# Kernel optimization log

Hardware: AMD Instinct MI355X
Metric: run time of the kernel (lower is better)

Reference implementation:

```python
import jax, jax.numpy as jnp
import numpy as np

N_NODES = 8192
N_EDGES = 65536
NB = 10            # number_of_basis
MID = 32           # middle_layer_size
MAX_R = 10.0       # max_radius
NZ, NM = 48, 16    # z / mol embedding sizes -> 64x0e node input
IN_S = NZ + NM     # 64 scalars
H_S, H_V = 32, 8   # hidden irreps 32x0e + 8x1o (dim 56)
O_S = 16           # output irreps 16x0e
W0N = IN_S * H_S + IN_S * H_V                                  # 2560
W1N = H_S*H_S + H_V*H_S + H_S*H_V + H_V*H_V + H_V*H_V          # 1664
W2N = H_S*O_S + H_V*O_S                                        # 640
H_DIM = H_S + 3 * H_V                                          # 56


def _fcnet(e, W1, W2):
    # e3nn FullyConnectedNet([NB, MID, numel], silu): fan-in normalized linears
    h = jax.nn.silu(e @ W1 / np.sqrt(W1.shape[0]))
    return h @ W2 / np.sqrt(W2.shape[0])


def _ln(x, g, b):
    m = jnp.mean(x, -1, keepdims=True)
    v = jnp.var(x, -1, keepdims=True)
    return (x - m) * jax.lax.rsqrt(v + 1e-5) * g + b


def _sus(t):
    # smooth compact-support bump helper: exp(-1/t) for t>0 else 0
    return jnp.where(t > 0, jnp.exp(-1.0 / jnp.where(t > 0, t, 1.0)), 0.0)


def _forward(pos, Ez, Em,
             b0_W1, b0_W2, b0_g, b0_b,
             b1_W1, b1_W2, b1_g, b1_b,
             b2_W1, b2_W2, b2_g, b2_b,
             z, mol_id, edge_src, edge_dst):
    N = pos.shape[0]
    E = edge_src.shape[0]
    avg = E / N  # avg_num_neighbors (static)

    # node embedding: 64x0e
    x = jnp.concatenate([Ez[z], Em[mol_id]], axis=-1)          # [N, 64]

    vec = pos[edge_dst] - pos[edge_src]                        # [E, 3]
    length = jnp.linalg.norm(vec, axis=1)                      # [E]

    # soft_one_hot_linspace(basis='smooth_finite', cutoff=True) * sqrt(NB)
    vals = jnp.linspace(0.0, MAX_R, NB + 2)[1:-1]
    step = MAX_R / (NB + 1)
    u = (length[:, None] - vals) / step
    emb = (1.14136 * np.exp(2.0)) * _sus(u + 1.0) * _sus(1.0 - u)
    emb = emb * np.sqrt(NB)                                    # [E, NB]

    # spherical harmonics lmax=1, normalize=True, 'component' norm
    nrm = vec / jnp.maximum(length, 1e-9)[:, None]
    sh_v = np.sqrt(3.0) * nrm                                  # [E, 3]  (l=1; l=0 comp == 1)

    # ---- interaction block 0: 64x0e -> 32x0e + 8x1o ----
    w = _fcnet(emb, b0_W1, b0_W2)                              # [E, 2560]
    w00 = w[:, :IN_S * H_S].reshape(E, IN_S, H_S)
    w01 = w[:, IN_S * H_S:].reshape(E, IN_S, H_V)
    xe = x[edge_src]                                           # [E, 64]
    es = jnp.einsum('eu,euw->ew', xe, w00) / np.sqrt(IN_S)
    ev = jnp.einsum('eu,euw,ei->ewi', xe, w01, sh_v) / np.sqrt(IN_S)
    msg = jnp.concatenate([es, ev.reshape(E, 3 * H_V)], -1)    # [E, 56]
    x = _ln(jax.ops.segment_sum(msg, edge_dst, num_segments=N) / np.sqrt(avg), b0_g, b0_b)

    # ---- interaction block 1: 32x0e+8x1o -> 32x0e+8x1o ----
    w = _fcnet(emb, b1_W1, b1_W2)                              # [E, 1664]
    o = 0
    w_ss  = w[:, o:o + H_S*H_S].reshape(E, H_S, H_S); o += H_S*H_S
    w_vvs = w[:, o:o + H_V*H_S].reshape(E, H_V, H_S); o += H_V*H_S
    w_sv  = w[:, o:o + H_S*H_V].reshape(E, H_S, H_V); o += H_S*H_V
    w_vs  = w[:, o:o + H_V*H_V].reshape(E, H_V, H_V); o += H_V*H_V
    w_vvv = w[:, o:o + H_V*H_V].reshape(E, H_V, H_V)
    xs = x[:, :H_S][edge_src]                                  # [E, 32]
    xv = x[:, H_S:].reshape(N, H_V, 3)[edge_src]               # [E, 8, 3]
    dot = jnp.einsum('eui,ei->eu', xv, sh_v) / np.sqrt(3.0)    # 1o x 1o -> 0e CG
    crs = jnp.cross(xv, sh_v[:, None, :]) / np.sqrt(2.0)       # 1o x 1o -> 1o CG
    es = (jnp.einsum('eu,euw->ew', xs, w_ss) / np.sqrt(H_S)
          + jnp.einsum('eu,euw->ew', dot, w_vvs) / np.sqrt(H_V)) / np.sqrt(2.0)
    ev = (jnp.einsum('eu,euw,ei->ewi', xs, w_sv, sh_v) / np.sqrt(H_S)
          + jnp.einsum('eui,euw->ewi', xv, w_vs) / np.sqrt(H_V)
          + jnp.einsum('eui,euw->ewi', crs, w_vvv) / np.sqrt(H_V)) / np.sqrt(3.0)
    msg = jnp.concatenate([es, ev.reshape(E, 3 * H_V)], -1)
    x = _ln(jax.ops.segment_sum(msg, edge_dst, num_segments=N) / np.sqrt(avg), b1_g, b1_b)

    # ---- interaction block 2: 32x0e+8x1o -> 16x0e ----
    w = _fcnet(emb, b2_W1, b2_W2)                              # [E, 640]
    w_ss  = w[:, :H_S * O_S].reshape(E, H_S, O_S)
    w_vvs = w[:, H_S * O_S:].reshape(E, H_V, O_S)
    xs = x[:, :H_S][edge_src]
    xv = x[:, H_S:].reshape(N, H_V, 3)[edge_src]
    dot = jnp.einsum('eui,ei->eu', xv, sh_v) / np.sqrt(3.0)
    es = (jnp.einsum('eu,euw->ew', xs, w_ss) / np.sqrt(H_S)
          + jnp.einsum('eu,euw->ew', dot, w_vvs) / np.sqrt(H_V)) / np.sqrt(2.0)
    x = _ln(jax.ops.segment_sum(es, edge_dst, num_segments=N) / np.sqrt(avg), b2_g, b2_b)
    return x                                                   # [N, 16]


def setup_inputs():
    key = jax.random.key(0)
    ks = jax.random.split(key, 16)
    edge_src = jax.random.randint(ks[3], (N_EDGES,), 0, N_NODES)
    # exclude self-loops (radius_graph never returns them)
    edge_dst = (edge_src + 1 + jax.random.randint(ks[4], (N_EDGES,), 0, N_NODES - 1)) % N_NODES
    return {
        'pos': jax.random.uniform(ks[0], (N_NODES, 3), jnp.float32) * 8.0,
        'z': jax.random.randint(ks[1], (N_NODES,), 0, 100),
        'mol_id': jax.random.randint(ks[2], (N_NODES,), 0, 2),
        'edge_src': edge_src,
        'edge_dst': edge_dst,
        'Ez': jax.random.normal(ks[5], (100, NZ), jnp.float32),
        'Em': jax.random.normal(ks[6], (2, NM), jnp.float32),
        'b0_W1': jax.random.normal(ks[7], (NB, MID), jnp.float32),
        'b0_W2': jax.random.normal(ks[8], (MID, W0N), jnp.float32),
        'b0_g': jnp.ones((H_DIM,), jnp.float32),
        'b0_b': jnp.zeros((H_DIM,), jnp.float32),
        'b1_W1': jax.random.normal(ks[9], (NB, MID), jnp.float32),
        'b1_W2': jax.random.normal(ks[10], (MID, W1N), jnp.float32),
        'b1_g': jnp.ones((H_DIM,), jnp.float32),
        'b1_b': jnp.zeros((H_DIM,), jnp.float32),
        'b2_W1': jax.random.normal(ks[11], (NB, MID), jnp.float32),
        'b2_W2': jax.random.normal(ks[12], (MID, W2N), jnp.float32),
        'b2_g': jnp.ones((O_S,), jnp.float32),
        'b2_b': jnp.zeros((O_S,), jnp.float32),
    }


def reference(pos, z, mol_id, edge_src, edge_dst, Ez, Em,
              b0_W1, b0_W2, b0_g, b0_b,
              b1_W1, b1_W2, b1_g, b1_b,
              b2_W1, b2_W2, b2_g, b2_b):
    return _forward(pos, Ez, Em,
                    b0_W1, b0_W2, b0_g, b0_b,
                    b1_W1, b1_W2, b1_g, b1_b,
                    b2_W1, b2_W2, b2_g, b2_b,
                    z, mol_id, edge_src, edge_dst)
```

## Files before the change

### kernel.cpp

```cpp
#include <hip/hip_runtime.h>

#define NNODES 8192
#define NEDGES 65536

#define K_PACK   0.02209708691f
#define K_P1SV   0.01804219593f
#define K_VVS    0.04419417382f
#define K_VS     0.03608439182f
#define K_VVV    0.02551551815f
#define K_DOT    0.57735026919f
#define K_PRELN  0.35355339059f
#define C_EMB    8.4335730689f

typedef unsigned int uint32;
typedef unsigned short ushort16;
typedef __attribute__((ext_vector_type(8))) short short8;
typedef __attribute__((ext_vector_type(4))) float floatx4;

__device__ __forceinline__ float siluf(float x) { return x / (1.0f + __expf(-x)); }
__device__ __forceinline__ float susf(float t) { return t > 0.0f ? __expf(-1.0f / t) : 0.0f; }
__device__ __forceinline__ ushort16 f2bf(float f) {
  uint32 u = __float_as_uint(f);
  return (ushort16)((u + 0x7fffu + ((u >> 16) & 1u)) >> 16);
}
__device__ __forceinline__ float bflo(uint32 v) { return __uint_as_float(v << 16); }
__device__ __forceinline__ float bfhi(uint32 v) { return __uint_as_float(v & 0xffff0000u); }
__device__ __forceinline__ float bfs(ushort16 v) { return __uint_as_float((uint32)v << 16); }

__global__ __launch_bounds__(256) void k_prep(
    const float* __restrict__ pos, const int* __restrict__ z, const int* __restrict__ mol,
    const int* __restrict__ esrc, const int* __restrict__ edst,
    const float* __restrict__ Ez, const float* __restrict__ Em,
    const float* __restrict__ W10, const float* __restrict__ W11, const float* __restrict__ W12,
    const float* __restrict__ W20, const float* __restrict__ W21, const float* __restrict__ W22,
    int* __restrict__ combo, ushort16* __restrict__ X0cb, float* __restrict__ sh,
    ushort16* __restrict__ h0b, ushort16* __restrict__ h1b, ushort16* __restrict__ h2b,
    ushort16* __restrict__ Bp0, ushort16* __restrict__ Bp1, ushort16* __restrict__ Bp2,
    ushort16* __restrict__ Bpw1, ushort16* __restrict__ Bpw2,
    int* __restrict__ deg, int* __restrict__ eidx) {
  __shared__ float Wl[320];
  int b = blockIdx.x;
  if (b < 768) {
    int which = b >> 8;
    int e = ((b & 255) << 8) + threadIdx.x;
    const float* W = (which == 0) ? W10 : (which == 1) ? W11 : W12;
    for (int i = threadIdx.x; i < 320; i += 256) Wl[i] = W[i];
    __syncthreads();
    int s = esrc[e], d = edst[e];
    float vx = pos[d * 3 + 0] - pos[s * 3 + 0];
    float vy = pos[d * 3 + 1] - pos[s * 3 + 1];
    float vz = pos[d * 3 + 2] - pos[s * 3 + 2];
    float len = sqrtf(vx * vx + vy * vy + vz * vz);
    if (which == 0) {
      int p = atomicAdd(&deg[d], 1);
      if (p < 64) eidx[(size_t)d * 64 + p] = e;
      float inv = 1.7320508076f / fmaxf(len, 1e-9f);
      sh[e * 3 + 0] = vx * inv; sh[e * 3 + 1] = vy * inv; sh[e * 3 + 2] = vz * inv;
    }
    float emb[10];
#pragma unroll
    for (int k = 0; k < 10; ++k) {
      float u = len * 1.1f - (float)(k + 1);
      emb[k] = C_EMB * susf(u + 1.0f) * susf(1.0f - u);
    }
    float H[32];
#pragma unroll
    for (int m = 0; m < 32; ++m) {
      float t = 0.f;
#pragma unroll
      for (int k = 0; k < 10; ++k) t += emb[k] * Wl[k * 32 + m];
      H[m] = siluf(t);
    }
    ushort16* hb = (which == 0) ? h0b : (which == 1) ? h1b : h2b;
    uint32* hp = (uint32*)(hb + (size_t)e * 32);
#pragma unroll
    for (int m = 0; m < 16; ++m)
      hp[m] = (uint32)f2bf(H[2 * m]) | ((uint32)f2bf(H[2 * m + 1]) << 16);
    return;
  }
  int idx = (b - 768) * 256 + threadIdx.x;
  if (idx < NNODES) { combo[idx] = z[idx] * 2 + mol[idx]; return; }
  idx -= NNODES;
  if (idx < 16384) {
    int c = idx >> 6, j = idx & 63;
    float v = 0.f;
    if (c < 200) {
      int zz = c >> 1, mm = c & 1;
      v = (j < 48) ? Ez[zz * 48 + j] : Em[mm * 16 + (j - 48)];
    }
    X0cb[idx] = f2bf(v);
    return;
  }
  idx -= 16384;
  if (idx < 81920) {
    int tile = idx >> 10; int r = idx & 1023;
    int kh = r >> 9; int rr = r & 511;
    int lane = rr >> 3, j = rr & 7;
    int k = kh * 32 + (lane >> 4) * 8 + j;
    int n = tile * 16 + (lane & 15);
    int c = n >> 5, m = n & 31;
    int col = (c < 32) ? (k * 32 + c) : (2048 + k * 8 + (c - 32));
    Bp0[idx] = f2bf(W20[m * 2560 + col] * K_PACK);
    return;
  }
  idx -= 81920;
  if (idx < 40960) {
    int tile = idx >> 9; int rr = idx & 511;
    int lane = rr >> 3, j = rr & 7;
    int k = (lane >> 4) * 8 + j;
    int n = tile * 16 + (lane & 15);
    int c = n >> 5, m = n & 31;
    float v = (c < 32) ? W21[m * 1664 + k * 32 + c] * K_PACK
                       : W21[m * 1664 + 1280 + k * 8 + (c - 32)] * K_P1SV;
    Bp1[idx] = f2bf(v);
    return;
  }
  idx -= 40960;
  if (idx < 16384) {
    int tile = idx >> 9; int rr = idx & 511;
    int lane = rr >> 3, j = rr & 7;
    int k = (lane >> 4) * 8 + j;
    int n = tile * 16 + (lane & 15);
    int c = n >> 5, m = n & 31;
    Bp2[idx] = f2bf(W22[m * 640 + k * 16 + c] * K_PACK);
    return;
  }
  idx -= 16384;
  if (idx < 12288) {
    int tile = idx >> 9; int rr = idx & 511;
    int lane = rr >> 3, j = rr & 7;
    int m = (lane >> 4) * 8 + j;
    int n = tile * 16 + (lane & 15);
    float v;
    if (n < 256) {
      int c = n >> 3, u = n & 7;
      v = W21[m * 1664 + 1024 + u * 32 + c] * K_VVS;
    } else if (n < 320) {
      int vo = (n - 256) >> 3, u = n & 7;
      v = W21[m * 1664 + 1536 + u * 8 + vo] * K_VS;
    } else {
      int vo = (n - 320) >> 3, u = n & 7;
      v = W21[m * 1664 + 1600 + u * 8 + vo] * K_VVV;
    }
    Bpw1[idx] = f2bf(v);
    return;
  }
  idx -= 12288;
  {
    int tile = idx >> 9; int rr = idx & 511;
    int lane = rr >> 3, j = rr & 7;
    int m = (lane >> 4) * 8 + j;
    int n = tile * 16 + (lane & 15);
    int c = n >> 3, u = n & 7;
    Bpw2[idx] = f2bf(W22[m * 640 + 512 + u * 16 + c] * K_VVS);
  }
}

__device__ __forceinline__ void gemm_tile(
    const ushort16* __restrict__ A, const ushort16* __restrict__ Bp, ushort16* __restrict__ C,
    int N, int K, int bx, int by, int wave, int lane) {
  int m0 = bx * 64 + wave * 16;
  int n0 = by * 64;
  int row = lane & 15, q = lane >> 4;
  int nkh = K >> 5;
  floatx4 acc[4];
  floatx4 zero = {0.f, 0.f, 0.f, 0.f};
#pragma unroll
  for (int t = 0; t < 4; ++t) acc[t] = zero;
  for (int kh = 0; kh < nkh; ++kh) {
    short8 a = *reinterpret_cast<const short8*>(A + (size_t)(m0 + row) * K + kh * 32 + q * 8);
#pragma unroll
    for (int t = 0; t < 4; ++t) {
      int T = (n0 >> 4) + t;
      short8 b = *reinterpret_cast<const short8*>(Bp + ((size_t)T * nkh + kh) * 512 + lane * 8);
      acc[t] = __builtin_amdgcn_mfma_f32_16x16x32_bf16(a, b, acc[t], 0, 0, 0);
    }
  }
  int colb = n0 + row;
#pragma unroll
  for (int t = 0; t < 4; ++t)
#pragma unroll
    for (int r = 0; r < 4; ++r)
      C[(size_t)(m0 + q * 4 + r) * N + colb + t * 16] = f2bf(acc[t][r]);
}

__global__ __launch_bounds__(256) void k_gemm_mfma(
    const ushort16* __restrict__ A, const ushort16* __restrict__ Bp, ushort16* __restrict__ C,
    int N, int K) {
  gemm_tile(A, Bp, C, N, K, blockIdx.x, blockIdx.y, threadIdx.x >> 6, threadIdx.x & 63);
}

__global__ __launch_bounds__(256) void k_gather0(
    const int* __restrict__ deg, const int* __restrict__ eidx,
    const int* __restrict__ combo, const int* __restrict__ esrc,
    const float* __restrict__ sh, const ushort16* __restrict__ hb,
    const ushort16* __restrict__ Pb,
    const float* __restrict__ g, const float* __restrict__ b,
    ushort16* __restrict__ xsb, float* __restrict__ xvf) {
  int n = __builtin_amdgcn_readfirstlane(blockIdx.x * 4 + (threadIdx.x >> 6));
  int lane = threadIdx.x & 63;
  int row = lane & 15, q = lane >> 4;
  int cnt = deg[n]; if (cnt > 64) cnt = 64;
  const int* ep = eidx + (size_t)n * 64;
  int lv = lane - 32;
  int vq = (lv >= 0) ? ((lv / 3 > 7) ? 7 : lv / 3) : 0;
  int vi = (lv >= 0) ? (lv - (lv / 3) * 3) : 0;
  int c2 = 32 + row; if (c2 > 39) c2 = 39;
  floatx4 zero = {0.f, 0.f, 0.f, 0.f};
  float v = 0.f;
  for (int j = 0; j < cnt; ++j) {
    int e = __builtin_amdgcn_readfirstlane(ep[j]);
    int s = __builtin_amdgcn_readfirstlane(esrc[e]);
    int rp = __builtin_amdgcn_readfirstlane(combo[s]);
    float sh0 = sh[e * 3 + 0], sh1 = sh[e * 3 + 1], sh2 = sh[e * 3 + 2];
    short8 af = *reinterpret_cast<const short8*>(hb + (size_t)e * 32 + q * 8);
    const ushort16* Pr = Pb + (size_t)rp * 1280;
    short8 bf0 = *reinterpret_cast<const short8*>(Pr + row * 32 + q * 8);
    short8 bf1 = *reinterpret_cast<const short8*>(Pr + (16 + row) * 32 + q * 8);
    short8 bf2 = *reinterpret_cast<const short8*>(Pr + c2 * 32 + q * 8);
    floatx4 p0 = __builtin_amdgcn_mfma_f32_16x16x32_bf16(af, bf0, zero, 0, 0, 0);
    floatx4 p1 = __builtin_amdgcn_mfma_f32_16x16x32_bf16(af, bf1, zero, 0, 0, 0);
    floatx4 p2 = __builtin_amdgcn_mfma_f32_16x16x32_bf16(af, bf2, zero, 0, 0, 0);
    float pv2 = __shfl(p2[0], vq, 64);
    float pdot = (lane < 16) ? p0[0] : (lane < 32) ? p1[0] : pv2;
    float mult = (lane < 32) ? 1.0f : ((vi == 0) ? sh0 : (vi == 1) ? sh1 : sh2);
    v += pdot * mult;
  }
  v *= K_PRELN;
  if (lane >= 56) v = 0.f;
  float sm = v, sq = v * v;
#pragma unroll
  for (int off = 32; off > 0; off >>= 1) {
    sm += __shfl_xor(sm, off, 64);
    sq += __shfl_xor(sq, off, 64);
  }
  float invD = 1.0f / 56.0f;
  float mean = sm * invD;
  float var = sq * invD - mean * mean;
  float rs = rsqrtf(var + 1e-5f);
  float r = (v - mean) * rs * g[lane < 56 ? lane : 0] + b[lane < 56 ? lane : 0];
  if (lane < 32) xsb[(size_t)n * 32 + lane] = f2bf(r);
  else if (lane < 56) xvf[(size_t)n * 24 + lane - 32] = r;
}

__global__ __launch_bounds__(256) void k_msg1f(
    const int* __restrict__ esrc, const float* __restrict__ sh, const ushort16* __restrict__ hb,
    const ushort16* __restrict__ Pb, const float* __restrict__ xv,
    const ushort16* __restrict__ Bpw, ushort16* __restrict__ msg) {
  __shared__ ushort16 Wlds[16][392];
  int w = threadIdx.x >> 6, lane = threadIdx.x & 63;
  int e0 = __builtin_amdgcn_readfirstlane(blockIdx.x * 16);
  int row = lane & 15, q = lane >> 4;
  short8 a1 = *reinterpret_cast<const short8*>(hb + (size_t)(e0 + row) * 32 + q * 8);
  floatx4 zero = {0.f, 0.f, 0.f, 0.f};
#pragma unroll
  for (int t6 = 0; t6 < 6; ++t6) {
    int T = w * 6 + t6;
    short8 b1 = *reinterpret_cast<const short8*>(Bpw + (size_t)T * 512 + lane * 8);
    floatx4 acc = __builtin_amdgcn_mfma_f32_16x16x32_bf16(a1, b1, zero, 0, 0, 0);
#pragma unroll
    for (int r = 0; r < 4; ++r)
      Wlds[q * 4 + r][T * 16 + row] = f2bf(acc[r]);
  }
  __syncthreads();
  int lv = lane - 32;
  int vq = (lv >= 0) ? ((lv / 3 > 7) ? 7 : lv / 3) : 0;
  int vi = (lv >= 0) ? (lv - (lv / 3) * 3) : 0;
  int c2 = 32 + row; if (c2 > 39) c2 = 39;
#pragma unroll
  for (int k = 0; k < 4; ++k) {
    int e = e0 + w * 4 + k;
    int s = __builtin_amdgcn_readfirstlane(esrc[e]);
    float sh0 = sh[e * 3 + 0], sh1 = sh[e * 3 + 1], sh2 = sh[e * 3 + 2];
    const float* xr = xv + (size_t)s * 24;
    const ushort16* wp = &Wlds[w * 4 + k][0];
    float vterm, mult;
    if (lane < 32) {
      mult = 1.0f;
      uint4 wv = *reinterpret_cast<const uint4*>(wp + lane * 8);
      float ww[8] = {bflo(wv.x), bfhi(wv.x), bflo(wv.y), bfhi(wv.y),
                     bflo(wv.z), bfhi(wv.z), bflo(wv.w), bfhi(wv.w)};
      vterm = 0.f;
#pragma unroll
      for (int u = 0; u < 8; ++u) {
        float du = K_DOT * (xr[u * 3] * sh0 + xr[u * 3 + 1] * sh1 + xr[u * 3 + 2] * sh2);
        vterm += du * ww[u];
      }
    } else {
      float shi = (vi == 0) ? sh0 : (vi == 1) ? sh1 : sh2;
      float s1 = (vi == 0) ? sh1 : (vi == 1) ? sh2 : sh0;
      float s2 = (vi == 0) ? sh2 : (vi == 1) ? sh0 : sh1;
      mult = shi;
      uint4 wvs = *reinterpret_cast<const uint4*>(wp + 256 + vq * 8);
      uint4 wvv = *reinterpret_cast<const uint4*>(wp + 320 + vq * 8);
      float vsw[8] = {bflo(wvs.x), bfhi(wvs.x), bflo(wvs.y), bfhi(wvs.y),
                      bflo(wvs.z), bfhi(wvs.z), bflo(wvs.w), bfhi(wvs.w)};
      float vvw[8] = {bflo(wvv.x), bfhi(wvv.x), bflo(wvv.y), bfhi(wvv.y),
                      bflo(wvv.z), bfhi(wvv.z), bflo(wvv.w), bfhi(wvv.w)};
      vterm = 0.f;
#pragma unroll
      for (int u = 0; u < 8; ++u) {
        float xu0 = xr[u * 3], xu1 = xr[u * 3 + 1], xu2 = xr[u * 3 + 2];
        float xui = (vi == 0) ? xu0 : (vi == 1) ? xu1 : xu2;
        float xi1 = (vi == 0) ? xu1 : (vi == 1) ? xu2 : xu0;
        float xi2 = (vi == 0) ? xu2 : (vi == 1) ? xu0 : xu1;
        float crs = xi1 * s2 - xi2 * s1;
        vterm += xui * vsw[u] + crs * vvw[u];
      }
    }
    short8 af = *reinterpret_cast<const short8*>(hb + (size_t)e * 32 + q * 8);
    const ushort16* Pr = Pb + (size_t)s * 1280;
    short8 bf0 = *reinterpret_cast<const short8*>(Pr + row * 32 + q * 8);
    short8 bf1 = *reinterpret_cast<const short8*>(Pr + (16 + row) * 32 + q * 8);
    short8 bf2 = *reinterpret_cast<const short8*>(Pr + c2 * 32 + q * 8);
    floatx4 p0 = __builtin_amdgcn_mfma_f32_16x16x32_bf16(af, bf0, zero, 0, 0, 0);
    floatx4 p1 = __builtin_amdgcn_mfma_f32_16x16x32_bf16(af, bf1, zero, 0, 0, 0);
    floatx4 p2 = __builtin_amdgcn_mfma_f32_16x16x32_bf16(af, bf2, zero, 0, 0, 0);
    float pv2 = __shfl(p2[0], vq, 64);
    float pdot = (lane < 16) ? p0[0] : (lane < 32) ? p1[0] : pv2;
    if (lane < 56) msg[(size_t)e * 56 + lane] = f2bf(pdot * mult + vterm);
  }
}

__global__ __launch_bounds__(256) void k_msg2f(
    const int* __restrict__ esrc, const float* __restrict__ sh, const ushort16* __restrict__ hb,
    const ushort16* __restrict__ Pb, const float* __restrict__ xv,
    const ushort16* __restrict__ Bpw, ushort16* __restrict__ msg) {
  __shared__ ushort16 Wlds[16][136];
  int w = threadIdx.x >> 6, lane = threadIdx.x & 63;
  int e0 = __builtin_amdgcn_readfirstlane(blockIdx.x * 16);
  int row = lane & 15, q = lane >> 4;
  short8 a1 = *reinterpret_cast<const short8*>(hb + (size_t)(e0 + row) * 32 + q * 8);
  floatx4 zero = {0.f, 0.f, 0.f, 0.f};
#pragma unroll
  for (int t2 = 0; t2 < 2; ++t2) {
    int T = w * 2 + t2;
    short8 b1 = *reinterpret_cast<const short8*>(Bpw + (size_t)T * 512 + lane * 8);
    floatx4 acc = __builtin_amdgcn_mfma_f32_16x16x32_bf16(a1, b1, zero, 0, 0, 0);
#pragma unroll
    for (int r = 0; r < 4; ++r)
      Wlds[q * 4 + r][T * 16 + row] = f2bf(acc[r]);
  }
  __syncthreads();
  int cch = lane & 15;
#pragma unroll
  for (int k = 0; k < 4; ++k) {
    int e = e0 + w * 4 + k;
    int s = __builtin_amdgcn_readfirstlane(esrc[e]);
    float sh0 = sh[e * 3 + 0], sh1 = sh[e * 3 + 1], sh2 = sh[e * 3 + 2];
    const float* xr = xv + (size_t)s * 24;
    uint4 wv = *reinterpret_cast<const uint4*>(&Wlds[w * 4 + k][0] + cch * 8);
    float ww[8] = {bflo(wv.x), bfhi(wv.x), bflo(wv.y), bfhi(wv.y),
                   bflo(wv.z), bfhi(wv.z), bflo(wv.w), bfhi(wv.w)};
    float vterm = 0.f;
#pragma unroll
    for (int u = 0; u < 8; ++u) {
      float du = K_DOT * (xr[u * 3] * sh0 + xr[u * 3 + 1] * sh1 + xr[u * 3 + 2] * sh2);
      vterm += du * ww[u];
    }
    short8 af = *reinterpret_cast<const short8*>(hb + (size_t)e * 32 + q * 8);
    short8 bf = *reinterpret_cast<const short8*>(Pb + (size_t)s * 512 + row * 32 + q * 8);
    floatx4 p0 = __builtin_amdgcn_mfma_f32_16x16x32_bf16(af, bf, zero, 0, 0, 0);
    if (lane < 16) msg[(size_t)e * 16 + lane] = f2bf(p0[0] + vterm);
  }
}

__global__ __launch_bounds__(256) void k_gather_ln(
    const int* __restrict__ deg, const int* __restrict__ eidx,
    const ushort16* __restrict__ msg, int D,
    const float* __restrict__ g, const float* __restrict__ b,
    ushort16* __restrict__ xsb, float* __restrict__ xvf, float* __restrict__ outf) {
  int n = __builtin_amdgcn_readfirstlane(blockIdx.x * 4 + (threadIdx.x >> 6));
  int lane = threadIdx.x & 63;
  int cnt = deg[n]; if (cnt > 64) cnt = 64;
  const int* ep = eidx + (size_t)n * 64;
  float v = 0.f;
  for (int j = 0; j < cnt; ++j) {
    int e = ep[j];
    if (lane < D) v += bfs(msg[(size_t)e * D + lane]);
  }
  v *= K_PRELN;
  if (lane >= D) v = 0.f;
  float sm = v, sq = v * v;
#pragma unroll
  for (int off = 32; off > 0; off >>= 1) {
    sm += __shfl_xor(sm, off, 64);
    sq += __shfl_xor(sq, off, 64);
  }
  float invD = 1.0f / (float)D;
  float mean = sm * invD;
  float var = sq * invD - mean * mean;
  float rs = rsqrtf(var + 1e-5f);
  float r = (v - mean) * rs * g[lane < D ? lane : 0] + b[lane < D ? lane : 0];
  if (outf) {
    if (lane < D) outf[(size_t)n * D + lane] = r;
  } else {
    if (lane < 32) xsb[(size_t)n * 32 + lane] = f2bf(r);
    else if (lane < 56) xvf[(size_t)n * 24 + lane - 32] = r;
  }
}

extern "C" void kernel_launch(void* const* d_in, const int* in_sizes, int n_in,
                              void* d_out, int out_size, void* d_ws, size_t ws_size,
                              hipStream_t stream) {
  const float* pos = (const float*)d_in[0];
  const int* z = (const int*)d_in[1];
  const int* mol = (const int*)d_in[2];
  const int* esrc = (const int*)d_in[3];
  const int* edst = (const int*)d_in[4];
  const float* Ez = (const float*)d_in[5];
  const float* Em = (const float*)d_in[6];
  const float* b0W1 = (const float*)d_in[7];
  const float* b0W2 = (const float*)d_in[8];
  const float* b0g = (const float*)d_in[9];
  const float* b0b = (const float*)d_in[10];
  const float* b1W1 = (const float*)d_in[11];
  const float* b1W2 = (const float*)d_in[12];
  const float* b1g = (const float*)d_in[13];
  const float* b1b = (const float*)d_in[14];
  const float* b2W1 = (const float*)d_in[15];
  const float* b2W2 = (const float*)d_in[16];
  const float* b2g = (const float*)d_in[17];
  const float* b2b = (const float*)d_in[18];
  float* out = (float*)d_out;

  float* ws = (float*)d_ws;
  size_t o = 0;
  int* combo = (int*)(ws + o); o += NNODES;
  int* deg = (int*)(ws + o); o += NNODES;
  int* eidx = (int*)(ws + o); o += (size_t)NNODES * 64;
  ushort16* X0cb = (ushort16*)(ws + o); o += 8192;
  ushort16* xs1b = (ushort16*)(ws + o); o += 131072;
  float* xv1 = ws + o; o += (size_t)NNODES * 24;
  ushort16* h0b = (ushort16*)(ws + o); o += (size_t)NEDGES * 16;
  ushort16* h1b = (ushort16*)(ws + o); o += (size_t)NEDGES * 16;
  ushort16* h2b = (ushort16*)(ws + o); o += (size_t)NEDGES * 16;
  float* shb = ws + o; o += (size_t)NEDGES * 3;
  ushort16* Bp0 = (ushort16*)(ws + o); o += 40960;
  ushort16* Bp1 = (ushort16*)(ws + o); o += 20480;
  ushort16* Bp2 = (ushort16*)(ws + o); o += 8192;
  ushort16* Bpw1 = (ushort16*)(ws + o); o += 6144;
  ushort16* Bpw2 = (ushort16*)(ws + o); o += 2048;
  ushort16* P12 = (ushort16*)(ws + o); o += (size_t)NNODES * 640;
  ushort16* msgb = (ushort16*)(ws + o); o += (size_t)NEDGES * 28;

  ushort16* P0c = P12;
  ushort16* xs2b = xs1b;
  float* xv2 = xv1;
  ushort16* msg16 = msgb;

  hipMemsetAsync(deg, 0, NNODES * sizeof(int), stream);

  k_prep<<<1472, 256, 0, stream>>>(pos, z, mol, esrc, edst, Ez, Em,
                                   b0W1, b1W1, b2W1, b0W2, b1W2, b2W2,
                                   combo, X0cb, shb, h0b, h1b, h2b,
                                   Bp0, Bp1, Bp2, Bpw1, Bpw2, deg, eidx);

  k_gemm_mfma<<<dim3(4, 20), 256, 0, stream>>>(X0cb, Bp0, P0c, 1280, 64);
  k_gather0<<<2048, 256, 0, stream>>>(deg, eidx, combo, esrc, shb, h0b, P0c,
                                      b0g, b0b, xs1b, xv1);

  k_gemm_mfma<<<dim3(128, 20), 256, 0, stream>>>(xs1b, Bp1, P12, 1280, 32);
  k_msg1f<<<4096, 256, 0, stream>>>(esrc, shb, h1b, P12, xv1, Bpw1, msgb);
  k_gather_ln<<<2048, 256, 0, stream>>>(deg, eidx, msgb, 56, b1g, b1b, xs2b, xv2, nullptr);

  k_gemm_mfma<<<dim3(128, 8), 256, 0, stream>>>(xs2b, Bp2, P12, 512, 32);
  k_msg2f<<<4096, 256, 0, stream>>>(esrc, shb, h2b, P12, xv2, Bpw2, msg16);
  k_gather_ln<<<2048, 256, 0, stream>>>(deg, eidx, msg16, 16, b2g, b2b, nullptr, nullptr, out);
}
```

Measured before the change: 205.3 us.

## Fuse block-2 message computation into destination-node gather and layer norm

Replaces the per-edge k_msg2f kernel and the following k_gather_ln pass with one kernel, k_gather2. Each wave walks one destination node's incoming edges, computes each message in registers and accumulates it, then applies the final layer norm and writes the output. This removes the bf16 message buffer's write and re-read and one kernel launch. In exchange it adds eight small MFMAs per edge (the Bpw2 layout is repacked for this) and serialises per-node edge work inside a wave, where it was batched across edges before.

```diff
diff --git a/kernel.cpp b/kernel.cpp
--- a/kernel.cpp
+++ b/kernel.cpp
@@ -150,9 +150,8 @@
     int tile = idx >> 9; int rr = idx & 511;
     int lane = rr >> 3, j = rr & 7;
     int m = (lane >> 4) * 8 + j;
-    int n = tile * 16 + (lane & 15);
-    int c = n >> 3, u = n & 7;
-    Bpw2[idx] = f2bf(W22[m * 640 + 512 + u * 16 + c] * K_VVS);
+    int c = lane & 15;
+    Bpw2[idx] = f2bf(W22[m * 640 + 512 + tile * 16 + c] * K_VVS);
   }
 }
 
@@ -322,47 +321,57 @@
   }
 }
 
-__global__ __launch_bounds__(256) void k_msg2f(
-    const int* __restrict__ esrc, const float* __restrict__ sh, const ushort16* __restrict__ hb,
-    const ushort16* __restrict__ Pb, const float* __restrict__ xv,
-    const ushort16* __restrict__ Bpw, ushort16* __restrict__ msg) {
-  __shared__ ushort16 Wlds[16][136];
-  int w = threadIdx.x >> 6, lane = threadIdx.x & 63;
-  int e0 = __builtin_amdgcn_readfirstlane(blockIdx.x * 16);
+__global__ __launch_bounds__(256) void k_gather2(
+    const int* __restrict__ deg, const int* __restrict__ eidx,
+    const int* __restrict__ esrc, const float* __restrict__ sh,
+    const ushort16* __restrict__ hb, const ushort16* __restrict__ Pb,
+    const float* __restrict__ xv, const ushort16* __restrict__ Bpw,
+    const float* __restrict__ g, const float* __restrict__ b,
+    float* __restrict__ outf) {
+  int n = __builtin_amdgcn_readfirstlane(blockIdx.x * 4 + (threadIdx.x >> 6));
+  int lane = threadIdx.x & 63;
   int row = lane & 15, q = lane >> 4;
-  short8 a1 = *reinterpret_cast<const short8*>(hb + (size_t)(e0 + row) * 32 + q * 8);
+  int cnt = deg[n]; if (cnt > 64) cnt = 64;
+  const int* ep = eidx + (size_t)n * 64;
   floatx4 zero = {0.f, 0.f, 0.f, 0.f};
-#pragma unroll
-  for (int t2 = 0; t2 < 2; ++t2) {
-    int T = w * 2 + t2;
-    short8 b1 = *reinterpret_cast<const short8*>(Bpw + (size_t)T * 512 + lane * 8);
-    floatx4 acc = __builtin_amdgcn_mfma_f32_16x16x32_bf16(a1, b1, zero, 0, 0, 0);
-#pragma unroll
-    for (int r = 0; r < 4; ++r)
-      Wlds[q * 4 + r][T * 16 + row] = f2bf(acc[r]);
-  }
-  __syncthreads();
-  int cch = lane & 15;
-#pragma unroll
-  for (int k = 0; k < 4; ++k) {
-    int e = e0 + w * 4 + k;
+  short8 Bw[8];
+#pragma unroll
+  for (int u = 0; u < 8; ++u)
+    Bw[u] = *reinterpret_cast<const short8*>(Bpw + (size_t)u * 512 + lane * 8);
+  float v = 0.f;
+  for (int j = 0; j < cnt; ++j) {
+    int e = __builtin_amdgcn_readfirstlane(ep[j]);
     int s = __builtin_amdgcn_readfirstlane(esrc[e]);
     float sh0 = sh[e * 3 + 0], sh1 = sh[e * 3 + 1], sh2 = sh[e * 3 + 2];
     const float* xr = xv + (size_t)s * 24;
-    uint4 wv = *reinterpret_cast<const uint4*>(&Wlds[w * 4 + k][0] + cch * 8);
-    float ww[8] = {bflo(wv.x), bfhi(wv.x), bflo(wv.y), bfhi(wv.y),
-                   bflo(wv.z), bfhi(wv.z), bflo(wv.w), bfhi(wv.w)};
-    float vterm = 0.f;
-#pragma unroll
-    for (int u = 0; u < 8; ++u) {
-      float du = K_DOT * (xr[u * 3] * sh0 + xr[u * 3 + 1] * sh1 + xr[u * 3 + 2] * sh2);
-      vterm += du * ww[u];
-    }
+    float du[8];
+#pragma unroll
+    for (int u = 0; u < 8; ++u)
+      du[u] = K_DOT * (xr[u * 3] * sh0 + xr[u * 3 + 1] * sh1 + xr[u * 3 + 2] * sh2);
     short8 af = *reinterpret_cast<const short8*>(hb + (size_t)e * 32 + q * 8);
     short8 bf = *reinterpret_cast<const short8*>(Pb + (size_t)s * 512 + row * 32 + q * 8);
     floatx4 p0 = __builtin_amdgcn_mfma_f32_16x16x32_bf16(af, bf, zero, 0, 0, 0);
-    if (lane < 16) msg[(size_t)e * 16 + lane] = f2bf(p0[0] + vterm);
-  }
+    float acc = p0[0];
+#pragma unroll
+    for (int u = 0; u < 8; ++u) {
+      floatx4 wD = __builtin_amdgcn_mfma_f32_16x16x32_bf16(af, Bw[u], zero, 0, 0, 0);
+      acc += du[u] * wD[0];
+    }
+    v += acc;
+  }
+  v *= K_PRELN;
+  float sm = v, sq = v * v;
+#pragma unroll
+  for (int off = 32; off > 0; off >>= 1) {
+    sm += __shfl_xor(sm, off, 64);
+    sq += __shfl_xor(sq, off, 64);
+  }
+  float invD = 1.0f / 64.0f;
+  float mean = sm * invD;
+  float var = sq * invD - mean * mean;
+  float rs = rsqrtf(var + 1e-5f);
+  float r = (v - mean) * rs * g[lane & 15] + b[lane & 15];
+  if (lane < 16) outf[(size_t)n * 16 + lane] = r;
 }
 
 __global__ __launch_bounds__(256) void k_gather_ln(
@@ -447,7 +456,6 @@
   ushort16* P0c = P12;
   ushort16* xs2b = xs1b;
   float* xv2 = xv1;
-  ushort16* msg16 = msgb;
 
   hipMemsetAsync(deg, 0, NNODES * sizeof(int), stream);
 
@@ -465,6 +473,6 @@
   k_gather_ln<<<2048, 256, 0, stream>>>(deg, eidx, msgb, 56, b1g, b1b, xs2b, xv2, nullptr);
 
   k_gemm_mfma<<<dim3(128, 8), 256, 0, stream>>>(xs2b, Bp2, P12, 512, 32);
-  k_msg2f<<<4096, 256, 0, stream>>>(esrc, shb, h2b, P12, xv2, Bpw2, msg16);
-  k_gather_ln<<<2048, 256, 0, stream>>>(deg, eidx, msg16, 16, b2g, b2b, nullptr, nullptr, out);
-}
+  k_gather2<<<2048, 256, 0, stream>>>(deg, eidx, esrc, shb, h2b, P12, xv2, Bpw2,
+                                      b2g, b2b, out);
+}
```

New measurement: 213.4 us. +3.9%, slower.
